# Performance work log

Measured on AMD Instinct MI355X. Metric: run time of the kernel, lower is better.

Reference implementation:

```python
import jax, jax.numpy as jnp
import numpy as np

NEG_INF = -1e30  # large negative for masking; avoids inf*0 NaNs under softmax


def setup_inputs() -> dict:
    key = jax.random.key(0)
    kq, kk, kv, kd = jax.random.split(key, 4)
    B, H, N, D = 1, 16, 4096, 64
    Q = jax.random.normal(kq, (B, H, N, D), dtype=jnp.float32)
    K = jax.random.normal(kk, (B, H, N, D), dtype=jnp.float32)
    V = jax.random.normal(kv, (B, H, N, D), dtype=jnp.float32)
    document_id = jnp.sort(jax.random.randint(kd, (N,), 0, 16, dtype=jnp.int32))
    return {"Q": Q, "K": K, "V": V, "document_id": document_id}


def reference(Q, K, V, document_id):
    # Q, K, V: [B, H, N, D]; document_id: [N]
    B, H, N, D = Q.shape
    scale = 1.0 / jnp.sqrt(jnp.float32(D))  # flex_attention default scaling
    # document mask: token pairs attend only within the same document
    mask = document_id[:, None] == document_id[None, :]  # [N, N] bool
    scores = jnp.einsum('bhqd,bhkd->bhqk', Q, K) * scale  # [B, H, N, N]
    scores = jnp.where(mask[None, None, :, :], scores, NEG_INF)
    probs = jax.nn.softmax(scores, axis=-1)
    out = jnp.einsum('bhqk,bhkd->bhqd', probs, V)  # [B, H, N, D]
    return out
```

## Files before the change

kernel.cpp:

```cpp
#include <hip/hip_runtime.h>
#include <hip/hip_bf16.h>

typedef __attribute__((ext_vector_type(8))) short short8;
typedef __attribute__((ext_vector_type(4))) float f32x4;
typedef __attribute__((ext_vector_type(4))) unsigned int u32x4;
typedef __attribute__((ext_vector_type(4))) unsigned short u16x4;
typedef unsigned short u16;

#define MFMA16 __builtin_amdgcn_mfma_f32_16x16x32_bf16

__device__ __forceinline__ u16 f2bf(float x) {
    unsigned int u = __builtin_bit_cast(unsigned int, x);
    u = (u + 0x7FFFu + ((u >> 16) & 1u)) >> 16;
    return (u16)u;
}

__device__ __forceinline__ void gll16(const void* g, void* l) {
    __builtin_amdgcn_global_load_lds(
        (const __attribute__((address_space(1))) unsigned int*)g,
        (__attribute__((address_space(3))) unsigned int*)l, 16, 0, 0);
}

constexpr int N_TOK = 4096;
constexpr int DH = 64;
constexpr int NH = 16;
constexpr float SCALE = 0.125f;
constexpr float SHIFT = 8.0f;
constexpr float MASKVAL = -1e30f;


__global__ __launch_bounds__(256)
void doc_prep3(const float* __restrict__ Kg, const float* __restrict__ Vg,
               const int* __restrict__ doc, u16* __restrict__ Kws,
               u16* __restrict__ Vws, int* __restrict__ bnds) {
    const int b = blockIdx.x;
    const int tid = threadIdx.x;
    if (b < 2048) {
        __shared__ u16 tile[DH][42];
        const int h = b >> 7, k0 = (b & 127) * 32;
        #pragma unroll
        for (int i = 0; i < 2; ++i) {
            const int idx = tid + i * 256;
            const int r = idx >> 4, c = (idx & 15) * 4;
            const float4 f = *(const float4*)&Vg[((size_t)h * N_TOK + k0 + r) * DH + c];
            tile[c + 0][r] = f2bf(f.x); tile[c + 1][r] = f2bf(f.y);
            tile[c + 2][r] = f2bf(f.z); tile[c + 3][r] = f2bf(f.w);
        }
        __syncthreads();
        #pragma unroll
        for (int i = 0; i < 2; ++i) {
            const int idx = tid + i * 256;
            const int d = idx >> 3, kq = (idx & 7) * 4;
            const int k = k0 + kq;
            const int q = (k & 31) >> 2;
            const int nk = (k & ~31) | ((((q >> 2) << 1) | (q & 1)) << 3)
                                     | (((q >> 1) & 1) << 2);
            const int sp = ((nk >> 3) & 15) ^ (d & 7);
            const int dstk = (sp << 3) | (nk & 7);
            u16x4 o;
            o[0] = tile[d][kq + 0]; o[1] = tile[d][kq + 1];
            o[2] = tile[d][kq + 2]; o[3] = tile[d][kq + 3];
            *(u16x4*)&Vws[((((size_t)h * 32 + (k >> 7)) * 64 + d) << 7) + dstk] = o;
        }
    } else if (b < 4096) {
        const int bb = b - 2048;
        const int h = bb >> 7, k0 = (bb & 127) * 32;
        #pragma unroll
        for (int i = 0; i < 2; ++i) {
            const int idx = tid + i * 256;
            const int r = idx >> 4, c = (idx & 15) * 4;
            const int k = k0 + r;
            const float4 f = *(const float4*)&Kg[((size_t)h * N_TOK + k) * DH + c];
            const int dstc = (((c >> 3) ^ (k & 7)) << 3) | (c & 7);
            u16x4 o;
            o[0] = f2bf(f.x); o[1] = f2bf(f.y); o[2] = f2bf(f.z); o[3] = f2bf(f.w);
            *(u16x4*)&Kws[(((size_t)h << 12) + k) * 64 + dstc] = o;
        }
    } else {
        if (tid < 17) bnds[tid] = N_TOK;
        __syncthreads();
        const int i0 = tid * 16;
        int prev = (i0 == 0) ? -1 : doc[i0 - 1];
        for (int j = 0; j < 16; ++j) {
            const int cur = doc[i0 + j];
            for (int dd = prev + 1; dd <= cur; ++dd) bnds[dd] = i0 + j;
            prev = cur;
        }
    }
}

__global__ __launch_bounds__(512, 2)
void doc_attn_v23(const float* __restrict__ Qg, const u16* __restrict__ Kws,
                  const u16* __restrict__ Vws, const int* __restrict__ bnds,
                  float* __restrict__ Out) {
    __shared__ __align__(16) u16 Ka[128 * 64];
    __shared__ __align__(16) u16 Kb[128 * 64];
    __shared__ __align__(16) u16 Va[64 * 128];
    __shared__ __align__(16) u16 Vb[64 * 128];

    const int bid = blockIdx.x;
    const int swz = ((bid & 7) << 6) | (bid >> 3);
    const int h = swz >> 5;
    const int dI = (swz >> 1) & 15;
    const int qh = swz & 1;
    const int tid = threadIdx.x;
    const int lane = tid & 63;
    const int w = tid >> 6;
    const int l15 = lane & 15;
    const int lg = lane >> 4;

    const int qs = bnds[dI], qe = bnds[dI + 1];
    const int len = qe - qs;
    if (len <= 0) return;
    const int nG = (len + 15) >> 4;
    const int nGh = (nG + 1) >> 1;
    const int gBeg = qh * nGh;
    const int gEnd = min(nG, gBeg + nGh);
    if (gBeg >= gEnd) return;

    const bool khsel = (lg >> 1) != 0;
    const int rsw = l15 & 7;

    const int C0beg = qs & ~127;

    auto issue = [&](int C0, u16* Kd, u16* Vd) {
        const char* ksrc = (const char*)(Kws + (((size_t)h << 12) + C0) * 64);
        const char* vsrc = (const char*)(Vws + ((((size_t)h * 32 + (C0 >> 7)) * 64) << 7));
        #pragma unroll
        for (int j = 0; j < 2; ++j) {
            const int seg = w * 2 + j;
            gll16(ksrc + seg * 1024 + lane * 16, (char*)Kd + seg * 1024);
            gll16(vsrc + seg * 1024 + lane * 16, (char*)Vd + seg * 1024);
        }
    };

    for (int p0 = gBeg; p0 < gEnd; p0 += 16) {
        issue(C0beg, Ka, Va);

        short8 aq[2][2];
        int gid[2];
        #pragma unroll
        for (int s = 0; s < 2; ++s) {
            const int g = p0 + w + 8 * s;
            gid[s] = (g < gEnd) ? g : -1;
            const int gl = (g < gEnd) ? g : 0;
            const int qrow = min(qs + gl * 16 + l15, N_TOK - 1);
            const float* qp = &Qg[((size_t)h * N_TOK + qrow) * DH + lg * 8];
            #pragma unroll
            for (int kc = 0; kc < 2; ++kc) {
                float4 f0 = *(const float4*)(qp + kc * 32);
                float4 f1 = *(const float4*)(qp + kc * 32 + 4);
                short8 a;
                a[0]=(short)f2bf(f0.x*SCALE); a[1]=(short)f2bf(f0.y*SCALE);
                a[2]=(short)f2bf(f0.z*SCALE); a[3]=(short)f2bf(f0.w*SCALE);
                a[4]=(short)f2bf(f1.x*SCALE); a[5]=(short)f2bf(f1.y*SCALE);
                a[6]=(short)f2bf(f1.z*SCALE); a[7]=(short)f2bf(f1.w*SCALE);
                aq[s][kc] = a;
            }
        }

        f32x4 o_acc[2][4];
        float lsum[2];
        #pragma unroll
        for (int s = 0; s < 2; ++s) {
            lsum[s] = 0.f;
            #pragma unroll
            for (int db = 0; db < 4; ++db) o_acc[s][db] = (f32x4){0.f, 0.f, 0.f, 0.f};
        }

        __syncthreads();

        u16 *Kc = Ka, *Vc = Va, *Kn = Kb, *Vn = Vb;
        for (int C0 = C0beg; C0 < qe; C0 += 128) {
            if (C0 + 128 < qe) issue(C0 + 128, Kn, Vn);

            const int t0 = (qs > C0) ? ((qs - C0) >> 5) : 0;
            int t1 = (qe - C0 + 31) >> 5; if (t1 > 4) t1 = 4;
            for (int t = t0; t < t1; ++t) {
                const int kb = t << 5;
                const int kabs = C0 + kb;
                short8 bk[2][2];
                #pragma unroll
                for (int kh = 0; kh < 2; ++kh)
                    #pragma unroll
                    for (int kc = 0; kc < 2; ++kc)
                        bk[kh][kc] = *(const short8*)&Kc[(size_t)(kb + kh * 16 + l15) * 64
                                            + (((lg + kc * 4) ^ rsw) << 3)];
                short8 bv[4];
                #pragma unroll
                for (int db = 0; db < 4; ++db)
                    bv[db] = *(const short8*)&Vc[(size_t)(db * 16 + l15) * 128
                                    + ((((kb >> 3) + lg) ^ rsw) << 3)];

                #pragma unroll
                for (int s = 0; s < 2; ++s) {
                    if (gid[s] < 0) continue;
                    f32x4 sa0 = (f32x4){-SHIFT, -SHIFT, -SHIFT, -SHIFT};
                    f32x4 sa1 = (f32x4){-SHIFT, -SHIFT, -SHIFT, -SHIFT};
                    __builtin_amdgcn_s_setprio(1);
                    sa0 = MFMA16(bk[0][0], aq[s][0], sa0, 0, 0, 0);
                    sa0 = MFMA16(bk[0][1], aq[s][1], sa0, 0, 0, 0);
                    sa1 = MFMA16(bk[1][0], aq[s][0], sa1, 0, 0, 0);
                    sa1 = MFMA16(bk[1][1], aq[s][1], sa1, 0, 0, 0);
                    __builtin_amdgcn_s_setprio(0);

                    float p0v[4], p1v[4];
                    #pragma unroll
                    for (int i = 0; i < 4; ++i) {
                        const int key0 = kabs + lg * 4 + i;
                        const int key1 = key0 + 16;
                        const float x0 = (key0 >= qs && key0 < qe) ? sa0[i] : MASKVAL;
                        const float x1 = (key1 >= qs && key1 < qe) ? sa1[i] : MASKVAL;
                        p0v[i] = __expf(x0);
                        p1v[i] = __expf(x1);
                        lsum[s] += p0v[i] + p1v[i];
                    }

                    const unsigned int a0 = (unsigned int)f2bf(p0v[0]) | ((unsigned int)f2bf(p0v[1]) << 16);
                    const unsigned int a1 = (unsigned int)f2bf(p0v[2]) | ((unsigned int)f2bf(p0v[3]) << 16);
                    const unsigned int b0w = (unsigned int)f2bf(p1v[0]) | ((unsigned int)f2bf(p1v[1]) << 16);
                    const unsigned int b1w = (unsigned int)f2bf(p1v[2]) | ((unsigned int)f2bf(p1v[3]) << 16);
                    const unsigned int aS0 = (unsigned int)__shfl_xor((int)a0, 32);
                    const unsigned int aS1 = (unsigned int)__shfl_xor((int)a1, 32);
                    const unsigned int bS0 = (unsigned int)__shfl_xor((int)b0w, 32);
                    const unsigned int bS1 = (unsigned int)__shfl_xor((int)b1w, 32);
                    u32x4 af;
                    af[0] = khsel ? bS0 : a0;
                    af[1] = khsel ? bS1 : a1;
                    af[2] = khsel ? b0w : aS0;
                    af[3] = khsel ? b1w : aS1;
                    const short8 pa = __builtin_bit_cast(short8, af);

                    __builtin_amdgcn_s_setprio(1);
                    #pragma unroll
                    for (int db = 0; db < 4; ++db)
                        o_acc[s][db] = MFMA16(bv[db], pa, o_acc[s][db], 0, 0, 0);
                    __builtin_amdgcn_s_setprio(0);
                }
            }

            __syncthreads();
            u16* tk = Kc; Kc = Kn; Kn = tk;
            u16* tv = Vc; Vc = Vn; Vn = tv;
        }

        #pragma unroll
        for (int s = 0; s < 2; ++s) {
            if (gid[s] < 0) continue;
            float rs = lsum[s];
            rs += __shfl_xor(rs, 16);
            rs += __shfl_xor(rs, 32);
            const float inv = 1.0f / rs;
            const int qrow = qs + gid[s] * 16 + l15;
            if (qrow < qe) {
                float* op = &Out[((size_t)h * N_TOK + qrow) * DH + lg * 4];
                #pragma unroll
                for (int db = 0; db < 4; ++db) {
                    float4 v;
                    v.x = o_acc[s][db][0] * inv;
                    v.y = o_acc[s][db][1] * inv;
                    v.z = o_acc[s][db][2] * inv;
                    v.w = o_acc[s][db][3] * inv;
                    *(float4*)(op + db * 16) = v;
                }
            }
        }
    }
}

constexpr int KMAXF = 128;
constexpr int KSTF = 72;
constexpr int VSTF = 136;

__global__ __launch_bounds__(512, 4)
void doc_attn_v16(const float* __restrict__ Qg, const float* __restrict__ Kg,
                  const float* __restrict__ Vg, const int* __restrict__ doc,
                  float* __restrict__ Out) {
    __shared__ __align__(16) u16 Klds[KMAXF][KSTF];
    __shared__ __align__(16) u16 Vtld[DH][VSTF];
    __shared__ int bnd[2];

    const int bid = blockIdx.x;
    const int swz = ((bid & 7) << 7) | (bid >> 3);
    const int h = swz >> 6;
    const int dI = (swz >> 2) & 15;
    const int qq = swz & 3;
    const int tid = threadIdx.x;
    const int lane = tid & 63;
    const int w = tid >> 6;
    const int l15 = lane & 15;
    const int lg = lane >> 4;

    if (tid == 0) { bnd[0] = N_TOK; bnd[1] = N_TOK; }
    __syncthreads();
    {
        const int i0 = tid * 8;
        int prev = (i0 == 0) ? -1 : doc[i0 - 1];
        #pragma unroll
        for (int j = 0; j < 8; ++j) {
            const int cur = doc[i0 + j];
            if (cur >= dI && prev < dI) bnd[0] = i0 + j;
            if (cur >= dI + 1 && prev < dI + 1) bnd[1] = i0 + j;
            prev = cur;
        }
    }
    __syncthreads();
    const int qs = bnd[0], qe = bnd[1];
    const int len = qe - qs;
    if (len <= 0) return;

    const int nG = (len + 15) >> 4;
    const int nGq = (nG + 3) >> 2;
    const int gBeg = qq * nGq;
    const int gEnd = min(nG, gBeg + nGq);
    if (gBeg >= gEnd) return;

    const int src0 = l15 + ((lane & 16) << 1);
    const int src1 = src0 + 16;
    const bool khsel = (lg >> 1) != 0;

    for (int g0 = gBeg; g0 < gEnd; g0 += 8) {
        const int g = g0 + w;
        const int gid = (g < gEnd) ? g : -1;
        short8 aq[2];
        {
            const int gl = (g < gEnd) ? g : 0;
            const int qrow = min(qs + gl * 16 + l15, N_TOK - 1);
            const float* qp = &Qg[((size_t)h * N_TOK + qrow) * DH + lg * 8];
            #pragma unroll
            for (int kc = 0; kc < 2; ++kc) {
                float4 f0 = *(const float4*)(qp + kc * 32);
                float4 f1 = *(const float4*)(qp + kc * 32 + 4);
                short8 a;
                a[0]=(short)f2bf(f0.x*SCALE); a[1]=(short)f2bf(f0.y*SCALE);
                a[2]=(short)f2bf(f0.z*SCALE); a[3]=(short)f2bf(f0.w*SCALE);
                a[4]=(short)f2bf(f1.x*SCALE); a[5]=(short)f2bf(f1.y*SCALE);
                a[6]=(short)f2bf(f1.z*SCALE); a[7]=(short)f2bf(f1.w*SCALE);
                aq[kc] = a;
            }
        }

        f32x4 o_acc[4];
        float lsum = 0.f;
        #pragma unroll
        for (int db = 0; db < 4; ++db) o_acc[db] = (f32x4){0.f, 0.f, 0.f, 0.f};

        for (int c0 = 0; c0 < len; c0 += KMAXF) {
            const int clen = min(KMAXF, len - c0);
            const int ctiles = (clen + 31) >> 5;
            const int cl32 = ctiles << 5;

            __syncthreads();

            for (int idx = tid; idx < clen * 16; idx += 512) {
                const int r = idx >> 4, c = (idx & 15) * 4;
                const float4 kf = *(const float4*)&Kg[((size_t)h * N_TOK + qs + c0 + r) * DH + c];
                const float4 vf = *(const float4*)&Vg[((size_t)h * N_TOK + qs + c0 + r) * DH + c];
                u16x4 o4;
                o4[0] = f2bf(kf.x); o4[1] = f2bf(kf.y);
                o4[2] = f2bf(kf.z); o4[3] = f2bf(kf.w);
                *(u16x4*)&Klds[r][c] = o4;
                Vtld[c + 0][r] = f2bf(vf.x);
                Vtld[c + 1][r] = f2bf(vf.y);
                Vtld[c + 2][r] = f2bf(vf.z);
                Vtld[c + 3][r] = f2bf(vf.w);
            }
            for (int idx = tid; idx < DH * 32; idx += 512) {
                const int d_ = idx >> 5;
                const int col = (clen & ~31) + (idx & 31);
                if (col >= clen && col < cl32) Vtld[d_][col] = 0;
            }
            __syncthreads();

            if (gid >= 0) {
                for (int t = 0; t < ctiles; ++t) {
                    const int kb = t << 5;
                    short8 bk[2][2];
                    #pragma unroll
                    for (int kh = 0; kh < 2; ++kh)
                        #pragma unroll
                        for (int kc = 0; kc < 2; ++kc)
                            bk[kh][kc] = *(const short8*)&Klds[kb + kh * 16 + l15][lg * 8 + kc * 32];

                    f32x4 sa0 = (f32x4){-SHIFT, -SHIFT, -SHIFT, -SHIFT};
                    f32x4 sa1 = (f32x4){-SHIFT, -SHIFT, -SHIFT, -SHIFT};
                    __builtin_amdgcn_s_setprio(1);
                    sa0 = MFMA16(bk[0][0], aq[0], sa0, 0, 0, 0);
                    sa0 = MFMA16(bk[0][1], aq[1], sa0, 0, 0, 0);
                    sa1 = MFMA16(bk[1][0], aq[0], sa1, 0, 0, 0);
                    sa1 = MFMA16(bk[1][1], aq[1], sa1, 0, 0, 0);
                    __builtin_amdgcn_s_setprio(0);

                    float p0[4], p1[4];
                    #pragma unroll
                    for (int i = 0; i < 4; ++i) {
                        const int key0 = kb + lg * 4 + i;
                        const float x0 = (key0 < clen)      ? sa0[i] : MASKVAL;
                        const float x1 = (key0 + 16 < clen) ? sa1[i] : MASKVAL;
                        p0[i] = __expf(x0);
                        p1[i] = __expf(x1);
                        lsum += p0[i] + p1[i];
                    }

                    const unsigned int a0 = (unsigned int)f2bf(p0[0]) | ((unsigned int)f2bf(p0[1]) << 16);
                    const unsigned int a1 = (unsigned int)f2bf(p0[2]) | ((unsigned int)f2bf(p0[3]) << 16);
                    const unsigned int b0w = (unsigned int)f2bf(p1[0]) | ((unsigned int)f2bf(p1[1]) << 16);
                    const unsigned int b1w = (unsigned int)f2bf(p1[2]) | ((unsigned int)f2bf(p1[3]) << 16);
                    const unsigned int t00 = __shfl((int)a0, src0);
                    const unsigned int t01 = __shfl((int)a1, src0);
                    const unsigned int t10 = __shfl((int)b0w, src0);
                    const unsigned int t11 = __shfl((int)b1w, src0);
                    const unsigned int u00 = __shfl((int)a0, src1);
                    const unsigned int u01 = __shfl((int)a1, src1);
                    const unsigned int u10 = __shfl((int)b0w, src1);
                    const unsigned int u11 = __shfl((int)b1w, src1);
                    u32x4 af;
                    af[0] = khsel ? t10 : t00;
                    af[1] = khsel ? t11 : t01;
                    af[2] = khsel ? u10 : u00;
                    af[3] = khsel ? u11 : u01;
                    const short8 pa = __builtin_bit_cast(short8, af);

                    short8 bv[4];
                    #pragma unroll
                    for (int db = 0; db < 4; ++db)
                        bv[db] = *(const short8*)&Vtld[db * 16 + l15][kb + lg * 8];

                    __builtin_amdgcn_s_setprio(1);
                    #pragma unroll
                    for (int db = 0; db < 4; ++db)
                        o_acc[db] = MFMA16(bv[db], pa, o_acc[db], 0, 0, 0);
                    __builtin_amdgcn_s_setprio(0);
                }
            }
        }

        if (gid >= 0) {
            float rs = lsum;
            rs += __shfl_xor(rs, 16);
            rs += __shfl_xor(rs, 32);
            const float inv = 1.0f / rs;
            const int qrow = qs + gid * 16 + l15;
            if (qrow < qe) {
                float* op = &Out[((size_t)h * N_TOK + qrow) * DH + lg * 4];
                #pragma unroll
                for (int db = 0; db < 4; ++db) {
                    float4 v;
                    v.x = o_acc[db][0] * inv;
                    v.y = o_acc[db][1] * inv;
                    v.z = o_acc[db][2] * inv;
                    v.w = o_acc[db][3] * inv;
                    *(float4*)(op + db * 16) = v;
                }
            }
        }
        lsum = 0.f;
    }
}

extern "C" void kernel_launch(void* const* d_in, const int* in_sizes, int n_in,
                              void* d_out, int out_size, void* d_ws, size_t ws_size,
                              hipStream_t stream) {
    const float* Q = (const float*)d_in[0];
    const float* K = (const float*)d_in[1];
    const float* V = (const float*)d_in[2];
    const int* doc = (const int*)d_in[3];
    float* out = (float*)d_out;

    const size_t kws_bytes = (size_t)NH * N_TOK * 64 * 2;
    const size_t vws_bytes = (size_t)NH * 32 * 64 * 128 * 2;
    const size_t bnds_off = kws_bytes + vws_bytes;
    const size_t need = bnds_off + 256;

    if (ws_size >= need) {
        u16* Kws = (u16*)d_ws;
        u16* Vws = (u16*)((char*)d_ws + kws_bytes);
        int* bnds = (int*)((char*)d_ws + bnds_off);
        doc_prep3<<<dim3(4097), 256, 0, stream>>>(K, V, doc, Kws, Vws, bnds);
        doc_attn_v23<<<dim3(512), 512, 0, stream>>>(Q, Kws, Vws, bnds, out);
    } else {
        doc_attn_v16<<<dim3(1024), 512, 0, stream>>>(Q, K, V, doc, out);
    }
}
```

Baseline: 40.58 us.

## Use one 1024-thread block per head-document with one query group per wave

The attention kernel no longer splits each (head, document) across two 512-thread blocks with two query groups per wave. It now launches one 1024-thread block per (head, document), with 16 waves each owning a single 16-row query group. Each K/V tile is staged into LDS once per document instead of twice, and each wave issues a single K and V global-to-LDS load. The cost is that register-held K/V fragments are reused across only one query group, so LDS reads per MFMA double. The grid halves to 256 blocks, and the `(1024, 4)` launch bound may tighten the register budget.

```diff
diff --git a/kernel.cpp b/kernel.cpp
--- a/kernel.cpp
+++ b/kernel.cpp
@@ -89,8 +89,8 @@
     }
 }
 
-__global__ __launch_bounds__(512, 2)
-void doc_attn_v23(const float* __restrict__ Qg, const u16* __restrict__ Kws,
+__global__ __launch_bounds__(1024, 4)
+void doc_attn_v24(const float* __restrict__ Qg, const u16* __restrict__ Kws,
                   const u16* __restrict__ Vws, const int* __restrict__ bnds,
                   float* __restrict__ Out) {
     __shared__ __align__(16) u16 Ka[128 * 64];
@@ -99,10 +99,9 @@
     __shared__ __align__(16) u16 Vb[64 * 128];
 
     const int bid = blockIdx.x;
-    const int swz = ((bid & 7) << 6) | (bid >> 3);
-    const int h = swz >> 5;
-    const int dI = (swz >> 1) & 15;
-    const int qh = swz & 1;
+    const int swz = ((bid & 7) << 5) | (bid >> 3);
+    const int h = swz >> 4;
+    const int dI = swz & 15;
     const int tid = threadIdx.x;
     const int lane = tid & 63;
     const int w = tid >> 6;
@@ -113,10 +112,6 @@
     const int len = qe - qs;
     if (len <= 0) return;
     const int nG = (len + 15) >> 4;
-    const int nGh = (nG + 1) >> 1;
-    const int gBeg = qh * nGh;
-    const int gEnd = min(nG, gBeg + nGh);
-    if (gBeg >= gEnd) return;
 
     const bool khsel = (lg >> 1) != 0;
     const int rsw = l15 & 7;
@@ -126,24 +121,19 @@
     auto issue = [&](int C0, u16* Kd, u16* Vd) {
         const char* ksrc = (const char*)(Kws + (((size_t)h << 12) + C0) * 64);
         const char* vsrc = (const char*)(Vws + ((((size_t)h * 32 + (C0 >> 7)) * 64) << 7));
-        #pragma unroll
-        for (int j = 0; j < 2; ++j) {
-            const int seg = w * 2 + j;
-            gll16(ksrc + seg * 1024 + lane * 16, (char*)Kd + seg * 1024);
-            gll16(vsrc + seg * 1024 + lane * 16, (char*)Vd + seg * 1024);
-        }
+        gll16(ksrc + w * 1024 + lane * 16, (char*)Kd + w * 1024);
+        gll16(vsrc + w * 1024 + lane * 16, (char*)Vd + w * 1024);
     };
 
-    for (int p0 = gBeg; p0 < gEnd; p0 += 16) {
+    for (int p0 = 0; p0 < nG; p0 += 16) {
+        const int g = p0 + w;
+        const int gid = (g < nG) ? g : -1;
+
         issue(C0beg, Ka, Va);
 
-        short8 aq[2][2];
-        int gid[2];
-        #pragma unroll
-        for (int s = 0; s < 2; ++s) {
-            const int g = p0 + w + 8 * s;
-            gid[s] = (g < gEnd) ? g : -1;
-            const int gl = (g < gEnd) ? g : 0;
+        short8 aq[2];
+        {
+            const int gl = (g < nG) ? g : 0;
             const int qrow = min(qs + gl * 16 + l15, N_TOK - 1);
             const float* qp = &Qg[((size_t)h * N_TOK + qrow) * DH + lg * 8];
             #pragma unroll
@@ -155,18 +145,14 @@
                 a[2]=(short)f2bf(f0.z*SCALE); a[3]=(short)f2bf(f0.w*SCALE);
                 a[4]=(short)f2bf(f1.x*SCALE); a[5]=(short)f2bf(f1.y*SCALE);
                 a[6]=(short)f2bf(f1.z*SCALE); a[7]=(short)f2bf(f1.w*SCALE);
-                aq[s][kc] = a;
-            }
-        }
-
-        f32x4 o_acc[2][4];
-        float lsum[2];
-        #pragma unroll
-        for (int s = 0; s < 2; ++s) {
-            lsum[s] = 0.f;
-            #pragma unroll
-            for (int db = 0; db < 4; ++db) o_acc[s][db] = (f32x4){0.f, 0.f, 0.f, 0.f};
-        }
+                aq[kc] = a;
+            }
+        }
+
+        f32x4 o_acc[4];
+        float lsum = 0.f;
+        #pragma unroll
+        for (int db = 0; db < 4; ++db) o_acc[db] = (f32x4){0.f, 0.f, 0.f, 0.f};
 
         __syncthreads();
 
@@ -176,32 +162,30 @@
 
             const int t0 = (qs > C0) ? ((qs - C0) >> 5) : 0;
             int t1 = (qe - C0 + 31) >> 5; if (t1 > 4) t1 = 4;
-            for (int t = t0; t < t1; ++t) {
-                const int kb = t << 5;
-                const int kabs = C0 + kb;
-                short8 bk[2][2];
-                #pragma unroll
-                for (int kh = 0; kh < 2; ++kh)
-                    #pragma unroll
-                    for (int kc = 0; kc < 2; ++kc)
-                        bk[kh][kc] = *(const short8*)&Kc[(size_t)(kb + kh * 16 + l15) * 64
-                                            + (((lg + kc * 4) ^ rsw) << 3)];
-                short8 bv[4];
-                #pragma unroll
-                for (int db = 0; db < 4; ++db)
-                    bv[db] = *(const short8*)&Vc[(size_t)(db * 16 + l15) * 128
-                                    + ((((kb >> 3) + lg) ^ rsw) << 3)];
-
-                #pragma unroll
-                for (int s = 0; s < 2; ++s) {
-                    if (gid[s] < 0) continue;
+            if (gid >= 0) {
+                for (int t = t0; t < t1; ++t) {
+                    const int kb = t << 5;
+                    const int kabs = C0 + kb;
+                    short8 bk[2][2];
+                    #pragma unroll
+                    for (int kh = 0; kh < 2; ++kh)
+                        #pragma unroll
+                        for (int kc = 0; kc < 2; ++kc)
+                            bk[kh][kc] = *(const short8*)&Kc[(size_t)(kb + kh * 16 + l15) * 64
+                                                + (((lg + kc * 4) ^ rsw) << 3)];
+                    short8 bv[4];
+                    #pragma unroll
+                    for (int db = 0; db < 4; ++db)
+                        bv[db] = *(const short8*)&Vc[(size_t)(db * 16 + l15) * 128
+                                        + ((((kb >> 3) + lg) ^ rsw) << 3)];
+
                     f32x4 sa0 = (f32x4){-SHIFT, -SHIFT, -SHIFT, -SHIFT};
                     f32x4 sa1 = (f32x4){-SHIFT, -SHIFT, -SHIFT, -SHIFT};
                     __builtin_amdgcn_s_setprio(1);
-                    sa0 = MFMA16(bk[0][0], aq[s][0], sa0, 0, 0, 0);
-                    sa0 = MFMA16(bk[0][1], aq[s][1], sa0, 0, 0, 0);
-                    sa1 = MFMA16(bk[1][0], aq[s][0], sa1, 0, 0, 0);
-                    sa1 = MFMA16(bk[1][1], aq[s][1], sa1, 0, 0, 0);
+                    sa0 = MFMA16(bk[0][0], aq[0], sa0, 0, 0, 0);
+                    sa0 = MFMA16(bk[0][1], aq[1], sa0, 0, 0, 0);
+                    sa1 = MFMA16(bk[1][0], aq[0], sa1, 0, 0, 0);
+                    sa1 = MFMA16(bk[1][1], aq[1], sa1, 0, 0, 0);
                     __builtin_amdgcn_s_setprio(0);
 
                     float p0v[4], p1v[4];
@@ -213,7 +197,7 @@
                         const float x1 = (key1 >= qs && key1 < qe) ? sa1[i] : MASKVAL;
                         p0v[i] = __expf(x0);
                         p1v[i] = __expf(x1);
-                        lsum[s] += p0v[i] + p1v[i];
+                        lsum += p0v[i] + p1v[i];
                     }
 
                     const unsigned int a0 = (unsigned int)f2bf(p0v[0]) | ((unsigned int)f2bf(p0v[1]) << 16);
@@ -234,7 +218,7 @@
                     __builtin_amdgcn_s_setprio(1);
                     #pragma unroll
                     for (int db = 0; db < 4; ++db)
-                        o_acc[s][db] = MFMA16(bv[db], pa, o_acc[s][db], 0, 0, 0);
+                        o_acc[db] = MFMA16(bv[db], pa, o_acc[db], 0, 0, 0);
                     __builtin_amdgcn_s_setprio(0);
                 }
             }
@@ -244,23 +228,21 @@
             u16* tv = Vc; Vc = Vn; Vn = tv;
         }
 
-        #pragma unroll
-        for (int s = 0; s < 2; ++s) {
-            if (gid[s] < 0) continue;
-            float rs = lsum[s];
+        if (gid >= 0) {
+            float rs = lsum;
             rs += __shfl_xor(rs, 16);
             rs += __shfl_xor(rs, 32);
             const float inv = 1.0f / rs;
-            const int qrow = qs + gid[s] * 16 + l15;
+            const int qrow = qs + gid * 16 + l15;
             if (qrow < qe) {
                 float* op = &Out[((size_t)h * N_TOK + qrow) * DH + lg * 4];
                 #pragma unroll
                 for (int db = 0; db < 4; ++db) {
                     float4 v;
-                    v.x = o_acc[s][db][0] * inv;
-                    v.y = o_acc[s][db][1] * inv;
-                    v.z = o_acc[s][db][2] * inv;
-                    v.w = o_acc[s][db][3] * inv;
+                    v.x = o_acc[db][0] * inv;
+                    v.y = o_acc[db][1] * inv;
+                    v.z = o_acc[db][2] * inv;
+                    v.w = o_acc[db][3] * inv;
                     *(float4*)(op + db * 16) = v;
                 }
             }
@@ -477,7 +459,7 @@
         u16* Vws = (u16*)((char*)d_ws + kws_bytes);
         int* bnds = (int*)((char*)d_ws + bnds_off);
         doc_prep3<<<dim3(4097), 256, 0, stream>>>(K, V, doc, Kws, Vws, bnds);
-        doc_attn_v23<<<dim3(512), 512, 0, stream>>>(Q, Kws, Vws, bnds, out);
+        doc_attn_v24<<<dim3(256), 1024, 0, stream>>>(Q, Kws, Vws, bnds, out);
     } else {
         doc_attn_v16<<<dim3(1024), 512, 0, stream>>>(Q, K, V, doc, out);
     }
```

After: 40.58 us. About the same (-0.0%).
